# Performance work log

Measured on AMD Instinct MI355X. Metric: run time of the kernel, lower is better.

Reference implementation:

```python
import jax, jax.numpy as jnp
import numpy as np

N_NODES = 100000
D = 128
N_EDGES = 640000


def _spmm(edge_index, w, x, n):
    # out[i] = sum over edges (i<-j): w * x[j]
    src, dst = edge_index[0], edge_index[1]
    return jax.ops.segment_sum(w[:, None] * x[dst], src, num_segments=n)


def setup_inputs() -> dict:
    key = jax.random.key(0)
    ks = jax.random.split(key, 8)
    inp = {
        "index_vectors": jax.random.normal(ks[0], (N_NODES, D), dtype=jnp.float32),
        "edge_index1": jax.random.randint(ks[1], (2, N_EDGES), 0, N_NODES, dtype=jnp.int64),
        "w1": jnp.ones((N_EDGES,), dtype=jnp.float32),
        "edge_index2": jax.random.randint(ks[2], (2, N_EDGES), 0, N_NODES, dtype=jnp.int64),
        "w2": jnp.ones((N_EDGES,), dtype=jnp.float32),
        "edge_index3": jax.random.randint(ks[3], (2, N_EDGES), 0, N_NODES, dtype=jnp.int64),
        "w3": jnp.ones((N_EDGES,), dtype=jnp.float32),
        "zeroth": jax.random.uniform(ks[4], (1, 1), dtype=jnp.float32),
        "fst": jax.random.uniform(ks[5], (1, 1), dtype=jnp.float32),
        "snd": jax.random.uniform(ks[6], (1, 1), dtype=jnp.float32),
        "trd": jax.random.uniform(ks[7], (1, 1), dtype=jnp.float32),
    }
    return inp


def reference(index_vectors, edge_index1, w1, edge_index2, w2, edge_index3, w3,
              zeroth, fst, snd, trd):
    n = index_vectors.shape[0]
    # hop-1 context: A @ x
    fst_ctx = _spmm(edge_index1, w1, index_vectors, n)
    # hop-2 context: A^2 @ roll(x, 1, axis=1)   (permute_vecs=True)
    snd_ctx = _spmm(edge_index2, w2, jnp.roll(index_vectors, 1, axis=1), n)
    # hop-3 context: A^3 @ roll(x, 2, axis=1)
    trd_ctx = _spmm(edge_index3, w3, jnp.roll(index_vectors, 2, axis=1), n)

    # relu-normalized scalar order weights (get_orders)
    r0, r1, r2, r3 = (jax.nn.relu(zeroth), jax.nn.relu(fst),
                      jax.nn.relu(snd), jax.nn.relu(trd))
    tot = r0 + r1 + r2 + r3 + 1e-6
    r0, r1, r2, r3 = r0 / tot, r1 / tot, r2 / tot, r3 / tot

    # use_sign=False -> plain weighted combination
    return r0 * index_vectors + r1 * fst_ctx + r2 * snd_ctx + r3 * trd_ctx
```

## Files before the change

### kernel.cpp

```cpp
#include <hip/hip_runtime.h>

#define N_NODES 100000
#define D 128
#define N_EDGES 640000
#define TOT_EDGES (3 * N_EDGES)

#define NB   1024
#define NPB  98
#define BCAP 2304
#define OVF_CAP 16384
#define EPB  3072
#define BINA_BLOCKS (TOT_EDGES / EPB)
#define EPT  (EPB / 256)
#define NKEY 512
#define CAST_BLOCKS ((N_NODES * D / 4 + 255) / 256)

#define WS_OVFCNT 0
#define WS_BCUR   64
#define WS_OVF    65600
#define WS_TMP    327744
#define WS_FREC   19202112
#define WS_OFFS   34562112
#define WS_XB     34962120
#define WS_TOTAL_FAST 60562120

#ifndef __has_builtin
#define __has_builtin(x) 0
#endif
#if __has_builtin(__builtin_amdgcn_alignbit)
#define ALIGN16(hi, lo) __builtin_amdgcn_alignbit((hi), (lo), 16)
#else
#define ALIGN16(hi, lo) (((hi) << 16) | ((lo) >> 16))
#endif

__device__ __forceinline__ void load_r(const float* z0, const float* z1,
                                       const float* z2, const float* z3,
                                       float& r0, float& r1, float& r2, float& r3) {
    r0 = fmaxf(z0[0], 0.0f);
    r1 = fmaxf(z1[0], 0.0f);
    r2 = fmaxf(z2[0], 0.0f);
    r3 = fmaxf(z3[0], 0.0f);
    float inv = 1.0f / (r0 + r1 + r2 + r3 + 1e-6f);
    r0 *= inv; r1 *= inv; r2 *= inv; r3 *= inv;
}

__device__ __forceinline__ unsigned short bf16rn(float f) {
    unsigned int u = __float_as_uint(f);
    u += 0x7FFFu + ((u >> 16) & 1u);
    return (unsigned short)(u >> 16);
}

__global__ __launch_bounds__(256) void prep_kernel(
        const float* __restrict__ x, ushort* __restrict__ xb,
        const int* __restrict__ ei1, const float* __restrict__ w1,
        const int* __restrict__ ei2, const float* __restrict__ w2,
        const int* __restrict__ ei3, const float* __restrict__ w3,
        const float* __restrict__ z0, const float* __restrict__ z1,
        const float* __restrict__ z2, const float* __restrict__ z3,
        int* __restrict__ bcur, int* __restrict__ ovf_count,
        int4* __restrict__ ovf, int2* __restrict__ tmp) {
    if (blockIdx.x >= BINA_BLOCKS) {
        int i = (blockIdx.x - BINA_BLOCKS) * 256 + threadIdx.x;
        if (i < N_NODES * D / 4) {
            float4 v = ((const float4*)x)[i];
            ushort4 h;
            h.x = bf16rn(v.x); h.y = bf16rn(v.y); h.z = bf16rn(v.z); h.w = bf16rn(v.w);
            ((ushort4*)xb)[i] = h;
        }
        return;
    }
    __shared__ int hist[NB];
    __shared__ int base[NB];
    int t = threadIdx.x;
    for (int i = t; i < NB; i += 256) hist[i] = 0;
    __syncthreads();

    float r0, r1, r2, r3;
    load_r(z0, z1, z2, z3, r0, r1, r2, r3);

    int e0 = blockIdx.x * EPB;
    int rank[EPT];
    int bkt[EPT];
    int rxv[EPT];
    float scv[EPT];

#pragma unroll
    for (int k = 0; k < EPT; ++k) {
        int e = e0 + t + k * 256;
        int set = e / N_EDGES;
        int idx = e - set * N_EDGES;
        const int* ei;  const float* w;  float rk;
        if      (set == 0) { ei = ei1; w = w1; rk = r1; }
        else if (set == 1) { ei = ei2; w = w2; rk = r2; }
        else               { ei = ei3; w = w3; rk = r3; }
        int src = ei[idx];
        int dst = ei[N_EDGES + idx];
        int b = src / NPB;
        int local = src - b * NPB;
        bkt[k]  = b;
        rxv[k]  = dst | (set << 17) | (local << 19);
        scv[k]  = rk * w[idx];
        rank[k] = atomicAdd(&hist[b], 1);
    }
    __syncthreads();

    for (int i = t; i < NB; i += 256) {
        int h = hist[i];
        base[i] = h ? atomicAdd(&bcur[i * 16], h) : 0;
    }
    __syncthreads();

#pragma unroll
    for (int k = 0; k < EPT; ++k) {
        int b = bkt[k];
        int pos = base[b] + rank[k];
        if (pos < BCAP) {
            tmp[(size_t)b * BCAP + pos] = make_int2(rxv[k], __float_as_int(scv[k]));
        } else {
            int o = atomicAdd(ovf_count, 1);
            int src = b * NPB + ((rxv[k] >> 19) & 0x7F);
            if (o < OVF_CAP) ovf[o] = make_int4(src, rxv[k] & 0x7FFFF,
                                                __float_as_int(scv[k]), 0);
        }
    }
}

__global__ __launch_bounds__(256) void binB_kernel(
        const int* __restrict__ bcur, const int2* __restrict__ tmp,
        int2* __restrict__ frecs, int* __restrict__ offsets) {
    __shared__ int sc4[256];
    __shared__ int d[NKEY];
    __shared__ int ts[256];
    __shared__ int cur[NKEY];
    __shared__ int sh_gbase, sh_n;
    int b = blockIdx.x;
    int t = threadIdx.x;

    d[t] = 0; d[t + 256] = 0;

    int v4[4];
    int cex[4];
    int tsum = 0;
#pragma unroll
    for (int k = 0; k < 4; ++k) {
        int g = 4 * t + k;
        int v = bcur[g * 16];
        if (v > BCAP) v = BCAP;
        cex[k] = tsum;
        tsum += v;
        v4[k] = v;
    }
    sc4[t] = tsum;
    __syncthreads();
    for (int off = 1; off < 256; off <<= 1) {
        int v = (t >= off) ? sc4[t - off] : 0;
        __syncthreads();
        sc4[t] += v;
        __syncthreads();
    }
    if (t == (b >> 2)) {
        sh_gbase = sc4[t] - tsum + cex[b & 3];
        sh_n     = v4[b & 3];
    }
    if (b == NB - 1 && t == 255) offsets[N_NODES] = sc4[255];
    __syncthreads();
    int gbase = sh_gbase;
    int n     = sh_n;

    for (int i = t; i < n; i += 256) {
        int rx = tmp[(size_t)b * BCAP + i].x;
        int key = (((rx >> 19) & 0x7F) << 2) | ((rx >> 17) & 3);
        atomicAdd(&d[key], 1);
    }
    __syncthreads();

    int k0 = d[2 * t], k1 = d[2 * t + 1];
    int tot = k0 + k1;
    ts[t] = tot;
    __syncthreads();
    for (int off = 1; off < 256; off <<= 1) {
        int v = (t >= off) ? ts[t - off] : 0;
        __syncthreads();
        ts[t] += v;
        __syncthreads();
    }
    int tbase = ts[t] - tot;
    cur[2 * t]     = tbase;
    cur[2 * t + 1] = tbase + k0;
    __syncthreads();

    if (t < NPB) {
        int node = b * NPB + t;
        if (node < N_NODES) offsets[node] = gbase + cur[t << 2];
    }
    __syncthreads();

    for (int i = t; i < n; i += 256) {
        int2 rec = tmp[(size_t)b * BCAP + i];
        int key = (((rec.x >> 19) & 0x7F) << 2) | ((rec.x >> 17) & 3);
        int pos = atomicAdd(&cur[key], 1);
        frecs[gbase + pos] = make_int2(rec.x & 0x7FFFF, rec.y);
    }
}

#define GB_ACC(V, RX, RY)                                                      \
    {                                                                          \
        int sh = ((RX) >> 17) & 3;                                             \
        float sc = __int_as_float(RY);                                         \
        unsigned int pw = (unsigned int)__shfl((int)(V).w, prevq);             \
        unsigned int s1x = ALIGN16((V).x, pw);                                 \
        unsigned int s1y = ALIGN16((V).y, (V).x);                              \
        unsigned int s1z = ALIGN16((V).z, (V).y);                              \
        unsigned int s1w = ALIGN16((V).w, (V).z);                              \
        unsigned int u0 = (sh == 0) ? (V).x : (sh == 1) ? s1x : pw;            \
        unsigned int u1 = (sh == 0) ? (V).y : (sh == 1) ? s1y : (V).x;         \
        unsigned int u2 = (sh == 0) ? (V).z : (sh == 1) ? s1z : (V).y;         \
        unsigned int u3 = (sh == 0) ? (V).w : (sh == 1) ? s1w : (V).z;         \
        acc0 += sc * __uint_as_float(u0 << 16);                                \
        acc1 += sc * __uint_as_float(u0 & 0xFFFF0000u);                        \
        acc2 += sc * __uint_as_float(u1 << 16);                                \
        acc3 += sc * __uint_as_float(u1 & 0xFFFF0000u);                        \
        acc4 += sc * __uint_as_float(u2 << 16);                                \
        acc5 += sc * __uint_as_float(u2 & 0xFFFF0000u);                        \
        acc6 += sc * __uint_as_float(u3 << 16);                                \
        acc7 += sc * __uint_as_float(u3 & 0xFFFF0000u);                        \
    }

__global__ __launch_bounds__(256) void gatherb_kernel(
        const float* __restrict__ x, const ushort* __restrict__ xb,
        const int* __restrict__ offsets, const int2* __restrict__ recs,
        const float* __restrict__ z0, const float* __restrict__ z1,
        const float* __restrict__ z2, const float* __restrict__ z3,
        float* __restrict__ out) {
    int wid  = (blockIdx.x * blockDim.x + threadIdx.x) >> 6;
    int lane = threadIdx.x & 63;
    if (wid >= N_NODES) return;

    float r0, r1, r2, r3;
    load_r(z0, z1, z2, z3, r0, r1, r2, r3);

    int qt    = lane >> 4;
    int l16   = lane & 15;
    int prevq = (qt << 4) | ((l16 + 15) & 15);

    int beg = offsets[wid];
    int end = offsets[wid + 1];
    int count = end - beg;
    int cnt64 = (count < 64) ? count : 64;

    int mrx = 0, mry = 0;
    if (lane < cnt64) { int2 rec = recs[beg + lane]; mrx = rec.x; mry = rec.y; }

    float acc0 = 0.f, acc1 = 0.f, acc2 = 0.f, acc3 = 0.f;
    float acc4 = 0.f, acc5 = 0.f, acc6 = 0.f, acc7 = 0.f;

    for (int j = 0; j < cnt64; j += 8) {
        int sa = j + qt;
        int sb = j + 4 + qt;
        int rxa = __shfl(mrx, sa), rya = __shfl(mry, sa);
        int rxb = __shfl(mrx, sb), ryb = __shfl(mry, sb);
        const uint4* pa = (const uint4*)(xb + (size_t)(rxa & 0x1FFFF) * D);
        const uint4* pb = (const uint4*)(xb + (size_t)(rxb & 0x1FFFF) * D);
        uint4 va = pa[l16];
        uint4 vb = pb[l16];
        GB_ACC(va, rxa, rya)
        GB_ACC(vb, rxb, ryb)
    }
    for (int q = 64; q < count; q += 4) {
        int qq = q + qt;
        int rx = 0, ry = 0;
        if (qq < count) { int2 rec = recs[beg + qq]; rx = rec.x; ry = rec.y; }
        const uint4* pp = (const uint4*)(xb + (size_t)(rx & 0x1FFFF) * D);
        uint4 vv = pp[l16];
        GB_ACC(vv, rx, ry)
    }

    acc0 += __shfl_xor(acc0, 16); acc0 += __shfl_xor(acc0, 32);
    acc1 += __shfl_xor(acc1, 16); acc1 += __shfl_xor(acc1, 32);
    acc2 += __shfl_xor(acc2, 16); acc2 += __shfl_xor(acc2, 32);
    acc3 += __shfl_xor(acc3, 16); acc3 += __shfl_xor(acc3, 32);
    acc4 += __shfl_xor(acc4, 16); acc4 += __shfl_xor(acc4, 32);
    acc5 += __shfl_xor(acc5, 16); acc5 += __shfl_xor(acc5, 32);
    acc6 += __shfl_xor(acc6, 16); acc6 += __shfl_xor(acc6, 32);
    acc7 += __shfl_xor(acc7, 16); acc7 += __shfl_xor(acc7, 32);

    if (lane < 16) {
        const float4* xr = (const float4*)(x + (size_t)wid * D);
        float4 xlo = xr[2 * l16];
        float4 xhi = xr[2 * l16 + 1];
        float4 olo, ohi;
        olo.x = r0 * xlo.x + acc0;
        olo.y = r0 * xlo.y + acc1;
        olo.z = r0 * xlo.z + acc2;
        olo.w = r0 * xlo.w + acc3;
        ohi.x = r0 * xhi.x + acc4;
        ohi.y = r0 * xhi.y + acc5;
        ohi.z = r0 * xhi.z + acc6;
        ohi.w = r0 * xhi.w + acc7;
        float4* op = (float4*)(out + (size_t)wid * D);
        op[2 * l16]     = olo;
        op[2 * l16 + 1] = ohi;
    }
}

__global__ void ovf_kernel(const float* __restrict__ x,
                           const int* __restrict__ ovf_count,
                           const int4* __restrict__ ovf,
                           float* __restrict__ out) {
    int total_waves = (gridDim.x * blockDim.x) >> 6;
    int gw   = (blockIdx.x * blockDim.x + threadIdx.x) >> 6;
    int lane = threadIdx.x & 63;
    int n = *ovf_count;
    if (n > OVF_CAP) n = OVF_CAP;
    for (int r = gw; r < n; r += total_waves) {
        int4 rec = ovf[r];
        int src = rec.x;
        int dst = rec.y & 0x1FFFF;
        int sh  = (rec.y >> 17) & 3;
        float sc = __int_as_float(rec.z);
        const float* xr = x + (size_t)dst * D;
        float* orow = out + (size_t)src * D;
        int c0 = 2 * lane, c1 = 2 * lane + 1;
        atomicAdd(&orow[c0], sc * xr[(c0 - sh) & 127]);
        atomicAdd(&orow[c1], sc * xr[(c1 - sh) & 127]);
    }
}

#define SCAN_BLOCKS ((N_NODES + 255) / 256)
#define WS_COUNTS   0
#define WS_OFFSETS  400000
#define WS_CURSORS  800008
#define WS_BSUM     1200008
#define WS_BPRE     1201576
#define WS_RECS     1203144
#define WS_NEEDED_MID (WS_RECS + (size_t)TOT_EDGES * 8)

__global__ void hist_kernel(const int* __restrict__ ei1, const int* __restrict__ ei2,
                            const int* __restrict__ ei3, int* __restrict__ counts) {
    int e = blockIdx.x * blockDim.x + threadIdx.x;
    if (e >= TOT_EDGES) return;
    int set = e / N_EDGES;
    int idx = e - set * N_EDGES;
    const int* ei = (set == 0) ? ei1 : (set == 1) ? ei2 : ei3;
    atomicAdd(&counts[ei[idx]], 1);
}

__global__ void scan1_kernel(const int* __restrict__ counts,
                             int* __restrict__ offsets, int* __restrict__ bsum) {
    __shared__ int s[256];
    int t = threadIdx.x;
    int i = blockIdx.x * 256 + t;
    int v = (i < N_NODES) ? counts[i] : 0;
    s[t] = v;
    __syncthreads();
    for (int off = 1; off < 256; off <<= 1) {
        int u = (t >= off) ? s[t - off] : 0;
        __syncthreads();
        s[t] += u;
        __syncthreads();
    }
    if (i < N_NODES) offsets[i] = s[t] - v;
    if (t == 255) bsum[blockIdx.x] = s[255];
}

__global__ void scan2_kernel(const int* __restrict__ bsum, int* __restrict__ bpre) {
    __shared__ int s[512];
    int t = threadIdx.x;
    int v = (t < SCAN_BLOCKS) ? bsum[t] : 0;
    s[t] = v;
    __syncthreads();
    for (int off = 1; off < 512; off <<= 1) {
        int u = (t >= off) ? s[t - off] : 0;
        __syncthreads();
        s[t] += u;
        __syncthreads();
    }
    if (t < SCAN_BLOCKS) bpre[t] = s[t] - v;
}

__global__ void scan3_kernel(int* __restrict__ offsets, const int* __restrict__ bpre,
                             int* __restrict__ cursors) {
    int i = blockIdx.x * 256 + threadIdx.x;
    if (i < N_NODES) {
        int v = offsets[i] + bpre[blockIdx.x];
        offsets[i] = v;
        cursors[i] = v;
    }
    if (i == 0) offsets[N_NODES] = TOT_EDGES;
}

__global__ void fill_kernel(const int* __restrict__ ei1, const float* __restrict__ w1,
                            const int* __restrict__ ei2, const float* __restrict__ w2,
                            const int* __restrict__ ei3, const float* __restrict__ w3,
                            const float* __restrict__ z0, const float* __restrict__ z1,
                            const float* __restrict__ z2, const float* __restrict__ z3,
                            int* __restrict__ cursors, int2* __restrict__ recs) {
    int e = blockIdx.x * blockDim.x + threadIdx.x;
    if (e >= TOT_EDGES) return;
    int set = e / N_EDGES;
    int idx = e - set * N_EDGES;
    const int* ei;  const float* w;
    if      (set == 0) { ei = ei1; w = w1; }
    else if (set == 1) { ei = ei2; w = w2; }
    else               { ei = ei3; w = w3; }
    float r0, r1, r2, r3;
    load_r(z0, z1, z2, z3, r0, r1, r2, r3);
    float rk = (set == 0) ? r1 : (set == 1) ? r2 : r3;
    int src = ei[idx];
    int dst = ei[N_EDGES + idx];
    float scale = rk * w[idx];
    int pos = atomicAdd(&cursors[src], 1);
    recs[pos] = make_int2(dst | (set << 17), __float_as_int(scale));
}

__global__ void gatherd_kernel(const float* __restrict__ x,
                               const int* __restrict__ offsets,
                               const int2* __restrict__ recs,
                               const float* __restrict__ z0, const float* __restrict__ z1,
                               const float* __restrict__ z2, const float* __restrict__ z3,
                               float* __restrict__ out) {
    int wid  = (blockIdx.x * blockDim.x + threadIdx.x) >> 6;
    int lane = threadIdx.x & 63;
    if (wid >= N_NODES) return;
    float r0, r1, r2, r3;
    load_r(z0, z1, z2, z3, r0, r1, r2, r3);
    float2 xv = ((const float2*)(x + (size_t)wid * D))[lane];
    int beg = offsets[wid];
    int end = offsets[wid + 1];
    float2 a0 = {0.f, 0.f}, a1 = {0.f, 0.f}, a2 = {0.f, 0.f};
    for (int j = beg; j < end; ++j) {
        int2 rec = recs[j];
        float2 v = ((const float2*)(x + (size_t)(rec.x & 0x1FFFF) * D))[lane];
        int sh = (rec.x >> 17) & 3;
        float sc = __int_as_float(rec.y);
        if      (sh == 0) { a0.x += sc * v.x; a0.y += sc * v.y; }
        else if (sh == 1) { a1.x += sc * v.x; a1.y += sc * v.y; }
        else               { a2.x += sc * v.x; a2.y += sc * v.y; }
    }
    int prev = (lane + 63) & 63;
    float r1y = __shfl(a1.y, prev);
    float r2x = __shfl(a2.x, prev);
    float r2y = __shfl(a2.y, prev);
    float2 o;
    o.x = r0 * xv.x + a0.x + r1y  + r2x;
    o.y = r0 * xv.y + a0.y + a1.x + r2y;
    ((float2*)(out + (size_t)wid * D))[lane] = o;
}

extern "C" void kernel_launch(void* const* d_in, const int* in_sizes, int n_in,
                              void* d_out, int out_size, void* d_ws, size_t ws_size,
                              hipStream_t stream) {
    const float* x   = (const float*)d_in[0];
    const int*   ei1 = (const int*)  d_in[1];
    const float* w1  = (const float*)d_in[2];
    const int*   ei2 = (const int*)  d_in[3];
    const float* w2  = (const float*)d_in[4];
    const int*   ei3 = (const int*)  d_in[5];
    const float* w3  = (const float*)d_in[6];
    const float* z0  = (const float*)d_in[7];
    const float* z1  = (const float*)d_in[8];
    const float* z2  = (const float*)d_in[9];
    const float* z3  = (const float*)d_in[10];
    float* out = (float*)d_out;
    char* wsc = (char*)d_ws;

    if (ws_size >= WS_TOTAL_FAST) {
        int*    ovf_count = (int*)   (wsc + WS_OVFCNT);
        int*    bcur      = (int*)   (wsc + WS_BCUR);
        int4*   ovf       = (int4*)  (wsc + WS_OVF);
        int2*   tmp       = (int2*)  (wsc + WS_TMP);
        int2*   frecs     = (int2*)  (wsc + WS_FREC);
        int*    offsets   = (int*)   (wsc + WS_OFFS);
        ushort* xb        = (ushort*)(wsc + WS_XB);

        hipMemsetAsync(wsc, 0, WS_OVF, stream);
        prep_kernel<<<BINA_BLOCKS + CAST_BLOCKS, 256, 0, stream>>>(
            x, xb, ei1, w1, ei2, w2, ei3, w3, z0, z1, z2, z3,
            bcur, ovf_count, ovf, tmp);
        binB_kernel<<<NB, 256, 0, stream>>>(bcur, tmp, frecs, offsets);
        gatherb_kernel<<<(N_NODES * 64 + 255) / 256, 256, 0, stream>>>(x, xb, offsets,
                                                                       frecs, z0, z1, z2, z3,
                                                                       out);
        ovf_kernel<<<128, 256, 0, stream>>>(x, ovf_count, ovf, out);
    } else {
        int*  counts  = (int*) (wsc + WS_COUNTS);
        int*  offsets = (int*) (wsc + WS_OFFSETS);
        int*  cursors = (int*) (wsc + WS_CURSORS);
        int*  bsum    = (int*) (wsc + WS_BSUM);
        int*  bpre    = (int*) (wsc + WS_BPRE);
        int2* recs    = (int2*)(wsc + WS_RECS);

        hipMemsetAsync(counts, 0, N_NODES * sizeof(int), stream);
        hist_kernel<<<TOT_EDGES / 256, 256, 0, stream>>>(ei1, ei2, ei3, counts);
        scan1_kernel<<<SCAN_BLOCKS, 256, 0, stream>>>(counts, offsets, bsum);
        scan2_kernel<<<1, 512, 0, stream>>>(bsum, bpre);
        scan3_kernel<<<SCAN_BLOCKS, 256, 0, stream>>>(offsets, bpre, cursors);
        fill_kernel<<<TOT_EDGES / 256, 256, 0, stream>>>(ei1, w1, ei2, w2, ei3, w3,
                                                         z0, z1, z2, z3, cursors, recs);
        gatherd_kernel<<<(N_NODES * 64 + 255) / 256, 256, 0, stream>>>(x, offsets, recs,
                                                                       z0, z1, z2, z3, out);
    }
}
```

Baseline: 282.1 us.

## Fuse bucket sort into gather kernel using shared-memory per-bucket records

Merges the second binning pass and the gather into one kernel. Each block loads its bucket's records into registers, counting-sorts them by (local node, set) into shared memory, then four waves gather bf16 rows for the bucket's 98 nodes. This removes the global frecs/offsets round trip and one launch. It also makes prep blocks single-set (EPB 2560) to drop per-edge set selection. In exchange, only 1024 blocks of 4 waves run the whole gather, which lowers parallelism and latency hiding, and the large shared-memory footprint limits occupancy.

After: 284.2 us. Within noise of the previous version (+0.7%).

```diff
diff --git a/kernel.cpp b/kernel.cpp
--- a/kernel.cpp
+++ b/kernel.cpp
@@ -8,9 +8,11 @@
 #define NB   1024
 #define NPB  98
 #define BCAP 2304
+#define RPT  9
 #define OVF_CAP 16384
-#define EPB  3072
+#define EPB  2560
 #define BINA_BLOCKS (TOT_EDGES / EPB)
+#define BLK_PER_SET (N_EDGES / EPB)
 #define EPT  (EPB / 256)
 #define NKEY 512
 #define CAST_BLOCKS ((N_NODES * D / 4 + 255) / 256)
@@ -78,7 +80,13 @@
     float r0, r1, r2, r3;
     load_r(z0, z1, z2, z3, r0, r1, r2, r3);
 
-    int e0 = blockIdx.x * EPB;
+    int set = blockIdx.x / BLK_PER_SET;
+    int e0  = (blockIdx.x - set * BLK_PER_SET) * EPB;
+    const int* ei;  const float* w;  float rk;
+    if      (set == 0) { ei = ei1; w = w1; rk = r1; }
+    else if (set == 1) { ei = ei2; w = w2; rk = r2; }
+    else               { ei = ei3; w = w3; rk = r3; }
+
     int rank[EPT];
     int bkt[EPT];
     int rxv[EPT];
@@ -86,13 +94,7 @@
 
 #pragma unroll
     for (int k = 0; k < EPT; ++k) {
-        int e = e0 + t + k * 256;
-        int set = e / N_EDGES;
-        int idx = e - set * N_EDGES;
-        const int* ei;  const float* w;  float rk;
-        if      (set == 0) { ei = ei1; w = w1; rk = r1; }
-        else if (set == 1) { ei = ei2; w = w2; rk = r2; }
-        else               { ei = ei3; w = w3; rk = r3; }
+        int idx = e0 + t + k * 256;
         int src = ei[idx];
         int dst = ei[N_EDGES + idx];
         int b = src / NPB;
@@ -125,88 +127,9 @@
     }
 }
 
-__global__ __launch_bounds__(256) void binB_kernel(
-        const int* __restrict__ bcur, const int2* __restrict__ tmp,
-        int2* __restrict__ frecs, int* __restrict__ offsets) {
-    __shared__ int sc4[256];
-    __shared__ int d[NKEY];
-    __shared__ int ts[256];
-    __shared__ int cur[NKEY];
-    __shared__ int sh_gbase, sh_n;
-    int b = blockIdx.x;
-    int t = threadIdx.x;
-
-    d[t] = 0; d[t + 256] = 0;
-
-    int v4[4];
-    int cex[4];
-    int tsum = 0;
-#pragma unroll
-    for (int k = 0; k < 4; ++k) {
-        int g = 4 * t + k;
-        int v = bcur[g * 16];
-        if (v > BCAP) v = BCAP;
-        cex[k] = tsum;
-        tsum += v;
-        v4[k] = v;
-    }
-    sc4[t] = tsum;
-    __syncthreads();
-    for (int off = 1; off < 256; off <<= 1) {
-        int v = (t >= off) ? sc4[t - off] : 0;
-        __syncthreads();
-        sc4[t] += v;
-        __syncthreads();
-    }
-    if (t == (b >> 2)) {
-        sh_gbase = sc4[t] - tsum + cex[b & 3];
-        sh_n     = v4[b & 3];
-    }
-    if (b == NB - 1 && t == 255) offsets[N_NODES] = sc4[255];
-    __syncthreads();
-    int gbase = sh_gbase;
-    int n     = sh_n;
-
-    for (int i = t; i < n; i += 256) {
-        int rx = tmp[(size_t)b * BCAP + i].x;
-        int key = (((rx >> 19) & 0x7F) << 2) | ((rx >> 17) & 3);
-        atomicAdd(&d[key], 1);
-    }
-    __syncthreads();
-
-    int k0 = d[2 * t], k1 = d[2 * t + 1];
-    int tot = k0 + k1;
-    ts[t] = tot;
-    __syncthreads();
-    for (int off = 1; off < 256; off <<= 1) {
-        int v = (t >= off) ? ts[t - off] : 0;
-        __syncthreads();
-        ts[t] += v;
-        __syncthreads();
-    }
-    int tbase = ts[t] - tot;
-    cur[2 * t]     = tbase;
-    cur[2 * t + 1] = tbase + k0;
-    __syncthreads();
-
-    if (t < NPB) {
-        int node = b * NPB + t;
-        if (node < N_NODES) offsets[node] = gbase + cur[t << 2];
-    }
-    __syncthreads();
-
-    for (int i = t; i < n; i += 256) {
-        int2 rec = tmp[(size_t)b * BCAP + i];
-        int key = (((rec.x >> 19) & 0x7F) << 2) | ((rec.x >> 17) & 3);
-        int pos = atomicAdd(&cur[key], 1);
-        frecs[gbase + pos] = make_int2(rec.x & 0x7FFFF, rec.y);
-    }
-}
-
-#define GB_ACC(V, RX, RY)                                                      \
+#define GB_ACC(V, RX, SC)                                                      \
     {                                                                          \
         int sh = ((RX) >> 17) & 3;                                             \
-        float sc = __int_as_float(RY);                                         \
         unsigned int pw = (unsigned int)__shfl((int)(V).w, prevq);             \
         unsigned int s1x = ALIGN16((V).x, pw);                                 \
         unsigned int s1y = ALIGN16((V).y, (V).x);                              \
@@ -216,90 +139,142 @@
         unsigned int u1 = (sh == 0) ? (V).y : (sh == 1) ? s1y : (V).x;         \
         unsigned int u2 = (sh == 0) ? (V).z : (sh == 1) ? s1z : (V).y;         \
         unsigned int u3 = (sh == 0) ? (V).w : (sh == 1) ? s1w : (V).z;         \
-        acc0 += sc * __uint_as_float(u0 << 16);                                \
-        acc1 += sc * __uint_as_float(u0 & 0xFFFF0000u);                        \
-        acc2 += sc * __uint_as_float(u1 << 16);                                \
-        acc3 += sc * __uint_as_float(u1 & 0xFFFF0000u);                        \
-        acc4 += sc * __uint_as_float(u2 << 16);                                \
-        acc5 += sc * __uint_as_float(u2 & 0xFFFF0000u);                        \
-        acc6 += sc * __uint_as_float(u3 << 16);                                \
-        acc7 += sc * __uint_as_float(u3 & 0xFFFF0000u);                        \
-    }
-
-__global__ __launch_bounds__(256) void gatherb_kernel(
+        acc0 += (SC) * __uint_as_float(u0 << 16);                              \
+        acc1 += (SC) * __uint_as_float(u0 & 0xFFFF0000u);                      \
+        acc2 += (SC) * __uint_as_float(u1 << 16);                              \
+        acc3 += (SC) * __uint_as_float(u1 & 0xFFFF0000u);                      \
+        acc4 += (SC) * __uint_as_float(u2 << 16);                              \
+        acc5 += (SC) * __uint_as_float(u2 & 0xFFFF0000u);                      \
+        acc6 += (SC) * __uint_as_float(u3 << 16);                              \
+        acc7 += (SC) * __uint_as_float(u3 & 0xFFFF0000u);                      \
+    }
+
+__global__ __launch_bounds__(256) void gfuse_kernel(
         const float* __restrict__ x, const ushort* __restrict__ xb,
-        const int* __restrict__ offsets, const int2* __restrict__ recs,
+        const int* __restrict__ bcur, const int2* __restrict__ tmp,
         const float* __restrict__ z0, const float* __restrict__ z1,
         const float* __restrict__ z2, const float* __restrict__ z3,
         float* __restrict__ out) {
-    int wid  = (blockIdx.x * blockDim.x + threadIdx.x) >> 6;
-    int lane = threadIdx.x & 63;
-    if (wid >= N_NODES) return;
+    __shared__ int2 srecs[BCAP];
+    __shared__ int d[NKEY];
+    __shared__ int ts[256];
+    __shared__ int cur[NKEY];
+    __shared__ int nodebeg[NPB + 1];
+
+    int b = blockIdx.x;
+    int t = threadIdx.x;
+
+    int n = bcur[b * 16];
+    if (n > BCAP) n = BCAP;
+
+    int   mrx[RPT];
+    int   mry[RPT];
+#pragma unroll
+    for (int k = 0; k < RPT; ++k) {
+        int i = t + k * 256;
+        if (i < n) {
+            int2 rec = tmp[(size_t)b * BCAP + i];
+            mrx[k] = rec.x; mry[k] = rec.y;
+        } else {
+            mrx[k] = -1; mry[k] = 0;
+        }
+    }
+
+    d[t] = 0; d[t + 256] = 0;
+    __syncthreads();
+#pragma unroll
+    for (int k = 0; k < RPT; ++k) {
+        if (mrx[k] != -1) {
+            int key = (((mrx[k] >> 19) & 0x7F) << 2) | ((mrx[k] >> 17) & 3);
+            atomicAdd(&d[key], 1);
+        }
+    }
+    __syncthreads();
+
+    int k0 = d[2 * t], k1 = d[2 * t + 1];
+    int tot = k0 + k1;
+    ts[t] = tot;
+    __syncthreads();
+    for (int off = 1; off < 256; off <<= 1) {
+        int v = (t >= off) ? ts[t - off] : 0;
+        __syncthreads();
+        ts[t] += v;
+        __syncthreads();
+    }
+    int tbase = ts[t] - tot;
+    cur[2 * t]     = tbase;
+    cur[2 * t + 1] = tbase + k0;
+    __syncthreads();
+
+    if (t < NPB) nodebeg[t] = cur[t << 2];
+    if (t == NPB) nodebeg[NPB] = n;
+    __syncthreads();
+
+#pragma unroll
+    for (int k = 0; k < RPT; ++k) {
+        if (mrx[k] != -1) {
+            int key = (((mrx[k] >> 19) & 0x7F) << 2) | ((mrx[k] >> 17) & 3);
+            int pos = atomicAdd(&cur[key], 1);
+            srecs[pos] = make_int2(mrx[k], mry[k]);
+        }
+    }
+    __syncthreads();
 
     float r0, r1, r2, r3;
     load_r(z0, z1, z2, z3, r0, r1, r2, r3);
 
+    int wv    = t >> 6;
+    int lane  = t & 63;
     int qt    = lane >> 4;
     int l16   = lane & 15;
     int prevq = (qt << 4) | ((l16 + 15) & 15);
 
-    int beg = offsets[wid];
-    int end = offsets[wid + 1];
-    int count = end - beg;
-    int cnt64 = (count < 64) ? count : 64;
-
-    int mrx = 0, mry = 0;
-    if (lane < cnt64) { int2 rec = recs[beg + lane]; mrx = rec.x; mry = rec.y; }
-
-    float acc0 = 0.f, acc1 = 0.f, acc2 = 0.f, acc3 = 0.f;
-    float acc4 = 0.f, acc5 = 0.f, acc6 = 0.f, acc7 = 0.f;
-
-    for (int j = 0; j < cnt64; j += 8) {
-        int sa = j + qt;
-        int sb = j + 4 + qt;
-        int rxa = __shfl(mrx, sa), rya = __shfl(mry, sa);
-        int rxb = __shfl(mrx, sb), ryb = __shfl(mry, sb);
-        const uint4* pa = (const uint4*)(xb + (size_t)(rxa & 0x1FFFF) * D);
-        const uint4* pb = (const uint4*)(xb + (size_t)(rxb & 0x1FFFF) * D);
-        uint4 va = pa[l16];
-        uint4 vb = pb[l16];
-        GB_ACC(va, rxa, rya)
-        GB_ACC(vb, rxb, ryb)
-    }
-    for (int q = 64; q < count; q += 4) {
-        int qq = q + qt;
-        int rx = 0, ry = 0;
-        if (qq < count) { int2 rec = recs[beg + qq]; rx = rec.x; ry = rec.y; }
-        const uint4* pp = (const uint4*)(xb + (size_t)(rx & 0x1FFFF) * D);
-        uint4 vv = pp[l16];
-        GB_ACC(vv, rx, ry)
-    }
-
-    acc0 += __shfl_xor(acc0, 16); acc0 += __shfl_xor(acc0, 32);
-    acc1 += __shfl_xor(acc1, 16); acc1 += __shfl_xor(acc1, 32);
-    acc2 += __shfl_xor(acc2, 16); acc2 += __shfl_xor(acc2, 32);
-    acc3 += __shfl_xor(acc3, 16); acc3 += __shfl_xor(acc3, 32);
-    acc4 += __shfl_xor(acc4, 16); acc4 += __shfl_xor(acc4, 32);
-    acc5 += __shfl_xor(acc5, 16); acc5 += __shfl_xor(acc5, 32);
-    acc6 += __shfl_xor(acc6, 16); acc6 += __shfl_xor(acc6, 32);
-    acc7 += __shfl_xor(acc7, 16); acc7 += __shfl_xor(acc7, 32);
-
-    if (lane < 16) {
-        const float4* xr = (const float4*)(x + (size_t)wid * D);
-        float4 xlo = xr[2 * l16];
-        float4 xhi = xr[2 * l16 + 1];
-        float4 olo, ohi;
-        olo.x = r0 * xlo.x + acc0;
-        olo.y = r0 * xlo.y + acc1;
-        olo.z = r0 * xlo.z + acc2;
-        olo.w = r0 * xlo.w + acc3;
-        ohi.x = r0 * xhi.x + acc4;
-        ohi.y = r0 * xhi.y + acc5;
-        ohi.z = r0 * xhi.z + acc6;
-        ohi.w = r0 * xhi.w + acc7;
-        float4* op = (float4*)(out + (size_t)wid * D);
-        op[2 * l16]     = olo;
-        op[2 * l16 + 1] = ohi;
+    for (int l = wv; l < NPB; l += 4) {
+        int node = b * NPB + l;
+        if (node >= N_NODES) break;
+        int beg = nodebeg[l];
+        int cnt = nodebeg[l + 1] - beg;
+
+        float acc0 = 0.f, acc1 = 0.f, acc2 = 0.f, acc3 = 0.f;
+        float acc4 = 0.f, acc5 = 0.f, acc6 = 0.f, acc7 = 0.f;
+
+        for (int j = 0; j < cnt; j += 4) {
+            int o = j + qt;
+            bool ok = o < cnt;
+            int2 rec = srecs[beg + (ok ? o : 0)];
+            int rx = rec.x;
+            float sc = ok ? __int_as_float(rec.y) : 0.f;
+            const uint4* rowp = (const uint4*)(xb + (size_t)(rx & 0x1FFFF) * D);
+            uint4 v = rowp[l16];
+            GB_ACC(v, rx, sc)
+        }
+
+        acc0 += __shfl_xor(acc0, 16); acc0 += __shfl_xor(acc0, 32);
+        acc1 += __shfl_xor(acc1, 16); acc1 += __shfl_xor(acc1, 32);
+        acc2 += __shfl_xor(acc2, 16); acc2 += __shfl_xor(acc2, 32);
+        acc3 += __shfl_xor(acc3, 16); acc3 += __shfl_xor(acc3, 32);
+        acc4 += __shfl_xor(acc4, 16); acc4 += __shfl_xor(acc4, 32);
+        acc5 += __shfl_xor(acc5, 16); acc5 += __shfl_xor(acc5, 32);
+        acc6 += __shfl_xor(acc6, 16); acc6 += __shfl_xor(acc6, 32);
+        acc7 += __shfl_xor(acc7, 16); acc7 += __shfl_xor(acc7, 32);
+
+        if (lane < 16) {
+            const float4* xr = (const float4*)(x + (size_t)node * D);
+            float4 xlo = xr[2 * l16];
+            float4 xhi = xr[2 * l16 + 1];
+            float4 olo, ohi;
+            olo.x = r0 * xlo.x + acc0;
+            olo.y = r0 * xlo.y + acc1;
+            olo.z = r0 * xlo.z + acc2;
+            olo.w = r0 * xlo.w + acc3;
+            ohi.x = r0 * xhi.x + acc4;
+            ohi.y = r0 * xhi.y + acc5;
+            ohi.z = r0 * xhi.z + acc6;
+            ohi.w = r0 * xhi.w + acc7;
+            float4* op = (float4*)(out + (size_t)node * D);
+            op[2 * l16]     = olo;
+            op[2 * l16 + 1] = ohi;
+        }
     }
 }
 
@@ -469,18 +444,14 @@
         int*    bcur      = (int*)   (wsc + WS_BCUR);
         int4*   ovf       = (int4*)  (wsc + WS_OVF);
         int2*   tmp       = (int2*)  (wsc + WS_TMP);
-        int2*   frecs     = (int2*)  (wsc + WS_FREC);
-        int*    offsets   = (int*)   (wsc + WS_OFFS);
         ushort* xb        = (ushort*)(wsc + WS_XB);
 
         hipMemsetAsync(wsc, 0, WS_OVF, stream);
         prep_kernel<<<BINA_BLOCKS + CAST_BLOCKS, 256, 0, stream>>>(
             x, xb, ei1, w1, ei2, w2, ei3, w3, z0, z1, z2, z3,
             bcur, ovf_count, ovf, tmp);
-        binB_kernel<<<NB, 256, 0, stream>>>(bcur, tmp, frecs, offsets);
-        gatherb_kernel<<<(N_NODES * 64 + 255) / 256, 256, 0, stream>>>(x, xb, offsets,
-                                                                       frecs, z0, z1, z2, z3,
-                                                                       out);
+        gfuse_kernel<<<NB, 256, 0, stream>>>(x, xb, bcur, tmp,
+                                             z0, z1, z2, z3, out);
         ovf_kernel<<<128, 256, 0, stream>>>(x, ovf_count, ovf, out);
     } else {
         int*  counts  = (int*) (wsc + WS_COUNTS);
```
